# Optimization experiments

Measured on AMD Instinct MI355X. Metric: run time of the kernel, lower is better.

Reference implementation:

```python
import jax, jax.numpy as jnp
import numpy as np

B, HG, WG, C, WH, WW, HEADS = 32, 8, 8, 256, 7, 7, 8
N = WH * WW  # 49 tokens per window


def _relative_index():
    # Mirrors the torch buffer construction exactly.
    coords = np.stack(np.meshgrid(np.arange(WH), np.arange(WW), indexing='ij'))  # [2, wh, ww]
    coords = coords.reshape(2, -1)                      # [2, N]
    rel = coords[:, :, None] - coords[:, None, :]       # [2, N, N]
    rel[0] += WH - 1
    rel[1] += WW - 1
    rel[0] *= 2 * WW - 1
    return rel.sum(0).reshape(-1).astype(np.int32)      # [N*N]


def setup_inputs() -> dict:
    key = jax.random.key(0)
    kx, kq, kp, kb = jax.random.split(key, 4)
    x = jax.random.normal(kx, (B, HG, WG, C, WH, WW), dtype=jnp.float32)
    qkv_w = jax.random.normal(kq, (3 * C, C), dtype=jnp.float32) * 0.02
    qkv_b = jnp.zeros((3 * C,), dtype=jnp.float32)
    proj_w = jax.random.normal(kp, (C, C), dtype=jnp.float32) * 0.02
    proj_b = jnp.zeros((C,), dtype=jnp.float32)
    bias_table = jax.random.normal(kb, ((2 * WH - 1) * (2 * WW - 1), HEADS), dtype=jnp.float32) * 0.02
    relative_index = jnp.asarray(_relative_index())
    return {"x": x, "qkv_w": qkv_w, "qkv_b": qkv_b, "proj_w": proj_w,
            "proj_b": proj_b, "bias_table": bias_table, "relative_index": relative_index}


def reference(x, qkv_w, qkv_b, proj_w, proj_b, bias_table, relative_index):
    Bq, Hg, Wg, Cc, wh, ww = x.shape
    n = wh * ww
    heads = bias_table.shape[1]
    hd = Cc // heads
    scale = hd ** -0.5

    xw = x.reshape(-1, Cc, n)                                   # [Bw, C, N]
    # 1x1 conv == channel matmul
    qkv = jnp.einsum('oc,bcn->bon', qkv_w, xw) + qkv_b[None, :, None]  # [Bw, 3C, N]
    q, k, v = jnp.split(qkv, 3, axis=1)

    def to_heads(t):  # [Bw, C, N] -> [Bw, heads, N, hd]
        return t.reshape(-1, heads, hd, n).transpose(0, 1, 3, 2)

    q, k, v = to_heads(q), to_heads(k), to_heads(v)

    # Gathered relative position bias: [heads, N, N]
    rel_bias = bias_table[relative_index].reshape(n, n, heads).transpose(2, 0, 1)

    attn = jnp.einsum('bhnd,bhmd->bhnm', q, k) * scale + rel_bias[None]
    attn = jax.nn.softmax(attn, axis=-1)
    out = jnp.einsum('bhnm,bhmd->bhnd', attn, v)                # [Bw, heads, N, hd]
    out = out.transpose(0, 1, 3, 2).reshape(-1, Cc, n)          # [Bw, C, N]
    out = jnp.einsum('oc,bcn->bon', proj_w, out) + proj_b[None, :, None]
    return out.reshape(Bq, Hg, Wg, Cc, wh, ww)
```

## Files before the change

kernel.cpp:

```cpp
#include <hip/hip_runtime.h>

typedef float f32x4 __attribute__((ext_vector_type(4)));
typedef short s16x8 __attribute__((ext_vector_type(8)));
typedef short s16x4 __attribute__((ext_vector_type(4)));

static __device__ __forceinline__ short f2b(float f) {
  unsigned u = __builtin_bit_cast(unsigned, f);
  u += 0x7fffu + ((u >> 16) & 1u);
  return (short)(u >> 16);
}

constexpr int kC  = 256;
constexpr int kN  = 49;
constexpr int kNP = 64;
constexpr int kHD = 32;
constexpr float kScale = 0.17677669529663687f;

constexpr int XT_P  = 264;
constexpr int QK_P  = 40;
constexpr int VT_P  = 72;
constexpr int P_P   = 72;
constexpr int AOT_P = 264;
constexpr int R1   = 64 * XT_P * 2;
constexpr int R2   = R1 + 8 * 64 * QK_P * 2;
constexpr int R3   = R2 + 8 * 64 * QK_P * 2;
constexpr int SMEM = R3 + 8 * 32 * VT_P * 2;

__global__ void prep_kernel(const float* __restrict__ qw,
                            const float* __restrict__ pw,
                            const float* __restrict__ bt,
                            const int* __restrict__ ri,
                            short* __restrict__ Wq,
                            short* __restrict__ Wp,
                            float* __restrict__ bx) {
  int i = blockIdx.x * 256 + threadIdx.x;
  if (i < 768 * 256) Wq[i] = f2b(qw[i]);
  if (i < 256 * 256) Wp[i] = f2b(pw[i]);
  if (i < 8 * 64 * 64) {
    int h = i >> 12, q = (i >> 6) & 63, k = i & 63;
    float v = -10000.f;
    if (q < kN && k < kN) v = bt[ri[q * kN + k] * 8 + h];
    bx[i] = v;
  }
}

__global__ __launch_bounds__(512, 2) void winattn_kernel(
    const float* __restrict__ x, const float* __restrict__ qkv_b,
    const float* __restrict__ proj_b, const short* __restrict__ Wq,
    const short* __restrict__ Wp, const float* __restrict__ biasx,
    float* __restrict__ out) {
  __shared__ alignas(16) char smem[SMEM];
  short* xT  = (short*)smem;
  short* aoT = xT;
  short* qs  = (short*)(smem + R1);
  short* ks  = (short*)(smem + R2);
  short* vt  = (short*)(smem + R3);

  const int tid  = threadIdx.x;
  const int wv   = tid >> 6;
  const int lane = tid & 63;
  const int lg   = lane >> 4;
  const int ln   = lane & 15;
  const size_t wbase = (size_t)blockIdx.x * (kC * kN);

  {
    const float* xw = x + wbase;
    for (int i = tid; i < kC * kN; i += 512) {
      int c = i / kN, n = i - c * kN;
      xT[n * XT_P + c] = f2b(xw[i]);
    }
    for (int i = tid; i < (kNP - kN) * kC; i += 512) {
      int n = kN + (i >> 8), c = i & 255;
      xT[n * XT_P + c] = 0;
    }
  }
  __syncthreads();

  {
    s16x8 Bf[4][8];
#pragma unroll
    for (int nt = 0; nt < 4; ++nt)
#pragma unroll
      for (int kk = 0; kk < 8; ++kk)
        Bf[nt][kk] = *(const s16x8*)&xT[(nt * 16 + ln) * XT_P + kk * 32 + lg * 8];

#pragma unroll 1
    for (int i = 0; i < 6; ++i) {
      const int mt = wv * 6 + i, o0 = mt * 16;
      const short* wr = Wq + (size_t)(o0 + ln) * kC;
      s16x8 Af[8];
#pragma unroll
      for (int kk = 0; kk < 8; ++kk) Af[kk] = *(const s16x8*)&wr[kk * 32 + lg * 8];
      f32x4 acc[4] = {};
#pragma unroll
      for (int kk = 0; kk < 8; ++kk)
#pragma unroll
        for (int nt = 0; nt < 4; ++nt)
          acc[nt] = __builtin_amdgcn_mfma_f32_16x16x32_bf16(Af[kk], Bf[nt][kk], acc[nt], 0, 0, 0);

      const int t = o0 >> 8, h = (o0 >> 5) & 7, d0 = (o0 & 31) + lg * 4;
      const f32x4 bq = *(const f32x4*)&qkv_b[o0 + lg * 4];
#pragma unroll
      for (int nt = 0; nt < 4; ++nt) {
        const int n = nt * 16 + ln;
        if (t < 2) {
          short* dst = (t == 0 ? qs : ks) + h * (kNP * QK_P) + n * QK_P + d0;
          s16x4 pk;
#pragma unroll
          for (int r = 0; r < 4; ++r) pk[r] = f2b(acc[nt][r] + bq[r]);
          *(s16x4*)dst = pk;
        } else {
#pragma unroll
          for (int r = 0; r < 4; ++r)
            vt[(h * kHD + d0 + r) * VT_P + n] = f2b(acc[nt][r] + bq[r]);
        }
      }
    }
  }
  __syncthreads();

  float Ssc[4][4][4];
  {
    const short* qh = qs + wv * (kNP * QK_P);
    const short* kh = ks + wv * (kNP * QK_P);
    s16x8 Qf[4], Kf[4];
#pragma unroll
    for (int tI = 0; tI < 4; ++tI) {
      Qf[tI] = *(const s16x8*)&qh[(tI * 16 + ln) * QK_P + lg * 8];
      Kf[tI] = *(const s16x8*)&kh[(tI * 16 + ln) * QK_P + lg * 8];
    }
    const float* bx = biasx + wv * (kNP * kNP);
#pragma unroll
    for (int qt = 0; qt < 4; ++qt)
#pragma unroll
      for (int nt = 0; nt < 4; ++nt) {
        f32x4 a = {};
        a = __builtin_amdgcn_mfma_f32_16x16x32_bf16(Qf[qt], Kf[nt], a, 0, 0, 0);
#pragma unroll
        for (int r = 0; r < 4; ++r) {
          const int qr = qt * 16 + lg * 4 + r;
          Ssc[qt][nt][r] = a[r] * kScale + bx[qr * kNP + nt * 16 + ln];
        }
      }
#pragma unroll
    for (int qt = 0; qt < 4; ++qt)
#pragma unroll
      for (int r = 0; r < 4; ++r) {
        float m = fmaxf(fmaxf(Ssc[qt][0][r], Ssc[qt][1][r]),
                        fmaxf(Ssc[qt][2][r], Ssc[qt][3][r]));
#pragma unroll
        for (int off = 1; off < 16; off <<= 1) m = fmaxf(m, __shfl_xor(m, off));
        float s = 0.f;
#pragma unroll
        for (int nt = 0; nt < 4; ++nt) {
          float p = __expf(Ssc[qt][nt][r] - m);
          Ssc[qt][nt][r] = p;
          s += p;
        }
#pragma unroll
        for (int off = 1; off < 16; off <<= 1) s += __shfl_xor(s, off);
        const float rinv = 1.f / s;
#pragma unroll
        for (int nt = 0; nt < 4; ++nt) Ssc[qt][nt][r] *= rinv;
      }
  }
  __syncthreads();

  short* Pw = qs + wv * (kNP * P_P);
#pragma unroll
  for (int qt = 0; qt < 4; ++qt)
#pragma unroll
    for (int nt = 0; nt < 4; ++nt)
#pragma unroll
      for (int r = 0; r < 4; ++r)
        Pw[(qt * 16 + lg * 4 + r) * P_P + nt * 16 + ln] = f2b(Ssc[qt][nt][r]);
  __syncthreads();

  {
    f32x4 O[4][2] = {};
#pragma unroll
    for (int kk = 0; kk < 2; ++kk) {
      s16x8 Vf[2];
#pragma unroll
      for (int dt = 0; dt < 2; ++dt)
        Vf[dt] = *(const s16x8*)&vt[(wv * kHD + dt * 16 + ln) * VT_P + kk * 32 + lg * 8];
#pragma unroll
      for (int qt = 0; qt < 4; ++qt) {
        const s16x8 Pf = *(const s16x8*)&Pw[(qt * 16 + ln) * P_P + kk * 32 + lg * 8];
#pragma unroll
        for (int dt = 0; dt < 2; ++dt)
          O[qt][dt] = __builtin_amdgcn_mfma_f32_16x16x32_bf16(Pf, Vf[dt], O[qt][dt], 0, 0, 0);
      }
    }
#pragma unroll
    for (int qt = 0; qt < 4; ++qt)
#pragma unroll
      for (int dt = 0; dt < 2; ++dt)
#pragma unroll
        for (int r = 0; r < 4; ++r)
          aoT[(qt * 16 + lg * 4 + r) * AOT_P + wv * kHD + dt * 16 + ln] = f2b(O[qt][dt][r]);
  }
  __syncthreads();

  {
    s16x8 Bp[4][8];
#pragma unroll
    for (int nt = 0; nt < 4; ++nt)
#pragma unroll
      for (int kk = 0; kk < 8; ++kk)
        Bp[nt][kk] = *(const s16x8*)&aoT[(nt * 16 + ln) * AOT_P + kk * 32 + lg * 8];

#pragma unroll 1
    for (int i = 0; i < 2; ++i) {
      const int mt = wv * 2 + i, o0 = mt * 16;
      const short* wr = Wp + (size_t)(o0 + ln) * kC;
      s16x8 Ap[8];
#pragma unroll
      for (int kk = 0; kk < 8; ++kk) Ap[kk] = *(const s16x8*)&wr[kk * 32 + lg * 8];
      f32x4 acc[4] = {};
#pragma unroll
      for (int kk = 0; kk < 8; ++kk)
#pragma unroll
        for (int nt = 0; nt < 4; ++nt)
          acc[nt] = __builtin_amdgcn_mfma_f32_16x16x32_bf16(Ap[kk], Bp[nt][kk], acc[nt], 0, 0, 0);

      const f32x4 pb = *(const f32x4*)&proj_b[o0 + lg * 4];
#pragma unroll
      for (int nt = 0; nt < 4; ++nt) {
        const int n = nt * 16 + ln;
        if (n < kN) {
#pragma unroll
          for (int r = 0; r < 4; ++r)
            out[wbase + (size_t)(o0 + lg * 4 + r) * kN + n] = acc[nt][r] + pb[r];
        }
      }
    }
  }
}

extern "C" void kernel_launch(void* const* d_in, const int* in_sizes, int n_in,
                              void* d_out, int out_size, void* d_ws, size_t ws_size,
                              hipStream_t stream) {
  (void)in_sizes; (void)n_in; (void)out_size; (void)ws_size;
  const float* x      = (const float*)d_in[0];
  const float* qkv_w  = (const float*)d_in[1];
  const float* qkv_b  = (const float*)d_in[2];
  const float* proj_w = (const float*)d_in[3];
  const float* proj_b = (const float*)d_in[4];
  const float* btab   = (const float*)d_in[5];
  const int*   ridx   = (const int*)d_in[6];

  short* Wq = (short*)d_ws;
  short* Wp = (short*)((char*)d_ws + 393216);
  float* bx = (float*)((char*)d_ws + 524288);

  prep_kernel<<<768, 256, 0, stream>>>(qkv_w, proj_w, btab, ridx, Wq, Wp, bx);
  winattn_kernel<<<2048, 512, 0, stream>>>(x, qkv_b, proj_b, Wq, Wp, bx, (float*)d_out);
}
```

Before: 233.9 us.

## Keep per-head Q/K/V and probabilities in registers via lane shuffles instead of LDS

Each wave now computes the Q, K and V projections for its own head directly. It turns the MFMA accumulators into operand fragments with packed bf16 conversion and lane shuffles, so the Q/K/V and P staging buffers in shared memory go away, along with their barriers. Shared memory shrinks to the single x/attention-output tile, and launch bounds rise to allow 4 blocks per CU. Softmax now uses transposed scores (K·Q with a transposed bias table) and applies normalization after the PV product. The risks are higher register pressure and repeated LDS reads of x per projection.

```diff
diff --git a/kernel.cpp b/kernel.cpp
--- a/kernel.cpp
+++ b/kernel.cpp
@@ -1,8 +1,9 @@
 #include <hip/hip_runtime.h>
 
-typedef float f32x4 __attribute__((ext_vector_type(4)));
-typedef short s16x8 __attribute__((ext_vector_type(8)));
-typedef short s16x4 __attribute__((ext_vector_type(4)));
+typedef float    f32x4 __attribute__((ext_vector_type(4)));
+typedef short    s16x8 __attribute__((ext_vector_type(8)));
+typedef short    s16x4 __attribute__((ext_vector_type(4)));
+typedef unsigned u32x4 __attribute__((ext_vector_type(4)));
 
 static __device__ __forceinline__ short f2b(float f) {
   unsigned u = __builtin_bit_cast(unsigned, f);
@@ -13,18 +14,10 @@
 constexpr int kC  = 256;
 constexpr int kN  = 49;
 constexpr int kNP = 64;
-constexpr int kHD = 32;
 constexpr float kScale = 0.17677669529663687f;
 
-constexpr int XT_P  = 264;
-constexpr int QK_P  = 40;
-constexpr int VT_P  = 72;
-constexpr int P_P   = 72;
-constexpr int AOT_P = 264;
-constexpr int R1   = 64 * XT_P * 2;
-constexpr int R2   = R1 + 8 * 64 * QK_P * 2;
-constexpr int R3   = R2 + 8 * 64 * QK_P * 2;
-constexpr int SMEM = R3 + 8 * 32 * VT_P * 2;
+constexpr int XT_P = 264;
+constexpr int SMEM = kNP * XT_P * 2;
 
 __global__ void prep_kernel(const float* __restrict__ qw,
                             const float* __restrict__ pw,
@@ -32,35 +25,51 @@
                             const int* __restrict__ ri,
                             short* __restrict__ Wq,
                             short* __restrict__ Wp,
-                            float* __restrict__ bx) {
+                            float* __restrict__ bxT) {
   int i = blockIdx.x * 256 + threadIdx.x;
   if (i < 768 * 256) Wq[i] = f2b(qw[i]);
   if (i < 256 * 256) Wp[i] = f2b(pw[i]);
   if (i < 8 * 64 * 64) {
-    int h = i >> 12, q = (i >> 6) & 63, k = i & 63;
+    int h = i >> 12, k = (i >> 6) & 63, q = i & 63;
     float v = -10000.f;
     if (q < kN && k < kN) v = bt[ri[q * kN + k] * 8 + h];
-    bx[i] = v;
-  }
-}
-
-__global__ __launch_bounds__(512, 2) void winattn_kernel(
+    bxT[i] = v;
+  }
+}
+
+static __device__ __forceinline__ s16x8 fragize(f32x4 Ta, f32x4 Tb, int hi, int srcbase) {
+  unsigned a0, a1, b0, b1;
+  asm("v_cvt_pk_bf16_f32 %0, %1, %2" : "=v"(a0) : "v"(Ta[0]), "v"(Ta[1]));
+  asm("v_cvt_pk_bf16_f32 %0, %1, %2" : "=v"(a1) : "v"(Ta[2]), "v"(Ta[3]));
+  asm("v_cvt_pk_bf16_f32 %0, %1, %2" : "=v"(b0) : "v"(Tb[0]), "v"(Tb[1]));
+  asm("v_cvt_pk_bf16_f32 %0, %1, %2" : "=v"(b1) : "v"(Tb[2]), "v"(Tb[3]));
+  u32x4 fw;
+#pragma unroll
+  for (int j = 0; j < 4; ++j) {
+    const int src = srcbase + (j >> 1) * 16;
+    unsigned wa = __shfl((j & 1) ? a1 : a0, src);
+    unsigned wb = __shfl((j & 1) ? b1 : b0, src);
+    fw[j] = hi ? wb : wa;
+  }
+  return __builtin_bit_cast(s16x8, fw);
+}
+
+__global__ __launch_bounds__(512, 4) void winattn_kernel(
     const float* __restrict__ x, const float* __restrict__ qkv_b,
     const float* __restrict__ proj_b, const short* __restrict__ Wq,
-    const short* __restrict__ Wp, const float* __restrict__ biasx,
+    const short* __restrict__ Wp, const float* __restrict__ bxT,
     float* __restrict__ out) {
   __shared__ alignas(16) char smem[SMEM];
   short* xT  = (short*)smem;
   short* aoT = xT;
-  short* qs  = (short*)(smem + R1);
-  short* ks  = (short*)(smem + R2);
-  short* vt  = (short*)(smem + R3);
 
   const int tid  = threadIdx.x;
   const int wv   = tid >> 6;
   const int lane = tid & 63;
   const int lg   = lane >> 4;
   const int ln   = lane & 15;
+  const int hi   = lg >> 1;
+  const int srcbase = (lg & 1) * 32 + ln;
   const size_t wbase = (size_t)blockIdx.x * (kC * kN);
 
   {
@@ -76,163 +85,184 @@
   }
   __syncthreads();
 
-  {
-    s16x8 Bf[4][8];
-#pragma unroll
-    for (int nt = 0; nt < 4; ++nt)
-#pragma unroll
-      for (int kk = 0; kk < 8; ++kk)
-        Bf[nt][kk] = *(const s16x8*)&xT[(nt * 16 + ln) * XT_P + kk * 32 + lg * 8];
+  s16x8 Qf[4], Kf[4], Vf[2][2];
+  {
+    f32x4 acc[2][4] = {};
+#pragma unroll
+    for (int kk = 0; kk < 8; ++kk) {
+      const s16x8 A0 = *(const s16x8*)&Wq[(size_t)(32 * wv + ln) * kC + kk * 32 + lg * 8];
+      const s16x8 A1 = *(const s16x8*)&Wq[(size_t)(32 * wv + 16 + ln) * kC + kk * 32 + lg * 8];
+      s16x8 B[4];
+#pragma unroll
+      for (int nt = 0; nt < 4; ++nt) B[nt] = *(const s16x8*)&xT[(nt * 16 + ln) * XT_P + kk * 32 + lg * 8];
+#pragma unroll
+      for (int nt = 0; nt < 4; ++nt) {
+        acc[0][nt] = __builtin_amdgcn_mfma_f32_16x16x32_bf16(A0, B[nt], acc[0][nt], 0, 0, 0);
+        acc[1][nt] = __builtin_amdgcn_mfma_f32_16x16x32_bf16(A1, B[nt], acc[1][nt], 0, 0, 0);
+      }
+    }
+    {
+      const f32x4 b0 = *(const f32x4*)&qkv_b[32 * wv + lg * 4];
+      const f32x4 b1 = *(const f32x4*)&qkv_b[32 * wv + 16 + lg * 4];
+#pragma unroll
+      for (int qt = 0; qt < 4; ++qt) {
+        f32x4 Ta, Tb;
+#pragma unroll
+        for (int r = 0; r < 4; ++r) {
+          Ta[r] = (acc[0][qt][r] + b0[r]) * kScale;
+          Tb[r] = (acc[1][qt][r] + b1[r]) * kScale;
+        }
+        Qf[qt] = fragize(Ta, Tb, hi, srcbase);
+      }
+    }
+#pragma unroll
+    for (int t = 0; t < 2; ++t)
+#pragma unroll
+      for (int nt = 0; nt < 4; ++nt) acc[t][nt] = f32x4{};
+#pragma unroll
+    for (int kk = 0; kk < 8; ++kk) {
+      const s16x8 A0 = *(const s16x8*)&Wq[(size_t)(256 + 32 * wv + ln) * kC + kk * 32 + lg * 8];
+      const s16x8 A1 = *(const s16x8*)&Wq[(size_t)(256 + 32 * wv + 16 + ln) * kC + kk * 32 + lg * 8];
+      s16x8 B[4];
+#pragma unroll
+      for (int nt = 0; nt < 4; ++nt) B[nt] = *(const s16x8*)&xT[(nt * 16 + ln) * XT_P + kk * 32 + lg * 8];
+#pragma unroll
+      for (int nt = 0; nt < 4; ++nt) {
+        acc[0][nt] = __builtin_amdgcn_mfma_f32_16x16x32_bf16(A0, B[nt], acc[0][nt], 0, 0, 0);
+        acc[1][nt] = __builtin_amdgcn_mfma_f32_16x16x32_bf16(A1, B[nt], acc[1][nt], 0, 0, 0);
+      }
+    }
+    {
+      const f32x4 b0 = *(const f32x4*)&qkv_b[256 + 32 * wv + lg * 4];
+      const f32x4 b1 = *(const f32x4*)&qkv_b[256 + 32 * wv + 16 + lg * 4];
+#pragma unroll
+      for (int qt = 0; qt < 4; ++qt) {
+        f32x4 Ta, Tb;
+#pragma unroll
+        for (int r = 0; r < 4; ++r) {
+          Ta[r] = acc[0][qt][r] + b0[r];
+          Tb[r] = acc[1][qt][r] + b1[r];
+        }
+        Kf[qt] = fragize(Ta, Tb, hi, srcbase);
+      }
+    }
+    f32x4 accv[4][2] = {};
+#pragma unroll
+    for (int kk = 0; kk < 8; ++kk) {
+      const s16x8 A0 = *(const s16x8*)&Wq[(size_t)(512 + 32 * wv + ln) * kC + kk * 32 + lg * 8];
+      const s16x8 A1 = *(const s16x8*)&Wq[(size_t)(512 + 32 * wv + 16 + ln) * kC + kk * 32 + lg * 8];
+      s16x8 B[4];
+#pragma unroll
+      for (int nt = 0; nt < 4; ++nt) B[nt] = *(const s16x8*)&xT[(nt * 16 + ln) * XT_P + kk * 32 + lg * 8];
+#pragma unroll
+      for (int tt = 0; tt < 4; ++tt) {
+        accv[tt][0] = __builtin_amdgcn_mfma_f32_16x16x32_bf16(B[tt], A0, accv[tt][0], 0, 0, 0);
+        accv[tt][1] = __builtin_amdgcn_mfma_f32_16x16x32_bf16(B[tt], A1, accv[tt][1], 0, 0, 0);
+      }
+    }
+    {
+      const float bv0 = qkv_b[512 + 32 * wv + ln];
+      const float bv1 = qkv_b[512 + 32 * wv + 16 + ln];
+#pragma unroll
+      for (int dt = 0; dt < 2; ++dt) {
+        const float bv = dt ? bv1 : bv0;
+#pragma unroll
+        for (int k2 = 0; k2 < 2; ++k2) {
+          f32x4 Ta, Tb;
+#pragma unroll
+          for (int r = 0; r < 4; ++r) {
+            Ta[r] = accv[2 * k2][dt][r] + bv;
+            Tb[r] = accv[2 * k2 + 1][dt][r] + bv;
+          }
+          Vf[dt][k2] = fragize(Ta, Tb, hi, srcbase);
+        }
+      }
+    }
+  }
+  __syncthreads();
+
+  s16x8 Pf[4][2];
+  float rinv[4];
+  {
+    const float* bxh = bxT + wv * (kNP * kNP);
+#pragma unroll
+    for (int qt = 0; qt < 4; ++qt) {
+      f32x4 S[4];
+#pragma unroll
+      for (int kt = 0; kt < 4; ++kt) {
+        f32x4 z = {};
+        S[kt] = __builtin_amdgcn_mfma_f32_16x16x32_bf16(Kf[kt], Qf[qt], z, 0, 0, 0);
+      }
+#pragma unroll
+      for (int kt = 0; kt < 4; ++kt)
+#pragma unroll
+        for (int r = 0; r < 4; ++r)
+          S[kt][r] += bxh[(kt * 16 + lg * 4 + r) * kNP + qt * 16 + ln];
+      float m = S[0][0];
+#pragma unroll
+      for (int kt = 0; kt < 4; ++kt)
+#pragma unroll
+        for (int r = 0; r < 4; ++r) m = fmaxf(m, S[kt][r]);
+      m = fmaxf(m, __shfl_xor(m, 16));
+      m = fmaxf(m, __shfl_xor(m, 32));
+      float s = 0.f;
+#pragma unroll
+      for (int kt = 0; kt < 4; ++kt)
+#pragma unroll
+        for (int r = 0; r < 4; ++r) {
+          float p = __expf(S[kt][r] - m);
+          S[kt][r] = p;
+          s += p;
+        }
+      s += __shfl_xor(s, 16);
+      s += __shfl_xor(s, 32);
+      rinv[qt] = 1.f / s;
+      Pf[qt][0] = fragize(S[0], S[1], hi, srcbase);
+      Pf[qt][1] = fragize(S[2], S[3], hi, srcbase);
+    }
+  }
+  {
+    f32x4 O[2][4] = {};
+#pragma unroll
+    for (int k2 = 0; k2 < 2; ++k2)
+#pragma unroll
+      for (int qt = 0; qt < 4; ++qt)
+#pragma unroll
+        for (int dt = 0; dt < 2; ++dt)
+          O[dt][qt] = __builtin_amdgcn_mfma_f32_16x16x32_bf16(Vf[dt][k2], Pf[qt][k2], O[dt][qt], 0, 0, 0);
+#pragma unroll
+    for (int dt = 0; dt < 2; ++dt)
+#pragma unroll
+      for (int qt = 0; qt < 4; ++qt) {
+        s16x4 pk;
+#pragma unroll
+        for (int r = 0; r < 4; ++r) pk[r] = f2b(O[dt][qt][r] * rinv[qt]);
+        *(s16x4*)&aoT[(qt * 16 + ln) * XT_P + wv * 32 + dt * 16 + lg * 4] = pk;
+      }
+  }
+  __syncthreads();
 
 #pragma unroll 1
-    for (int i = 0; i < 6; ++i) {
-      const int mt = wv * 6 + i, o0 = mt * 16;
-      const short* wr = Wq + (size_t)(o0 + ln) * kC;
-      s16x8 Af[8];
-#pragma unroll
-      for (int kk = 0; kk < 8; ++kk) Af[kk] = *(const s16x8*)&wr[kk * 32 + lg * 8];
-      f32x4 acc[4] = {};
-#pragma unroll
-      for (int kk = 0; kk < 8; ++kk)
-#pragma unroll
-        for (int nt = 0; nt < 4; ++nt)
-          acc[nt] = __builtin_amdgcn_mfma_f32_16x16x32_bf16(Af[kk], Bf[nt][kk], acc[nt], 0, 0, 0);
-
-      const int t = o0 >> 8, h = (o0 >> 5) & 7, d0 = (o0 & 31) + lg * 4;
-      const f32x4 bq = *(const f32x4*)&qkv_b[o0 + lg * 4];
+  for (int i = 0; i < 2; ++i) {
+    const int o0 = 32 * wv + 16 * i;
+    f32x4 acc[4] = {};
+#pragma unroll
+    for (int kk = 0; kk < 8; ++kk) {
+      const s16x8 A = *(const s16x8*)&Wp[(size_t)(o0 + ln) * kC + kk * 32 + lg * 8];
 #pragma unroll
       for (int nt = 0; nt < 4; ++nt) {
-        const int n = nt * 16 + ln;
-        if (t < 2) {
-          short* dst = (t == 0 ? qs : ks) + h * (kNP * QK_P) + n * QK_P + d0;
-          s16x4 pk;
-#pragma unroll
-          for (int r = 0; r < 4; ++r) pk[r] = f2b(acc[nt][r] + bq[r]);
-          *(s16x4*)dst = pk;
-        } else {
-#pragma unroll
-          for (int r = 0; r < 4; ++r)
-            vt[(h * kHD + d0 + r) * VT_P + n] = f2b(acc[nt][r] + bq[r]);
-        }
-      }
-    }
-  }
-  __syncthreads();
-
-  float Ssc[4][4][4];
-  {
-    const short* qh = qs + wv * (kNP * QK_P);
-    const short* kh = ks + wv * (kNP * QK_P);
-    s16x8 Qf[4], Kf[4];
-#pragma unroll
-    for (int tI = 0; tI < 4; ++tI) {
-      Qf[tI] = *(const s16x8*)&qh[(tI * 16 + ln) * QK_P + lg * 8];
-      Kf[tI] = *(const s16x8*)&kh[(tI * 16 + ln) * QK_P + lg * 8];
-    }
-    const float* bx = biasx + wv * (kNP * kNP);
-#pragma unroll
-    for (int qt = 0; qt < 4; ++qt)
-#pragma unroll
-      for (int nt = 0; nt < 4; ++nt) {
-        f32x4 a = {};
-        a = __builtin_amdgcn_mfma_f32_16x16x32_bf16(Qf[qt], Kf[nt], a, 0, 0, 0);
-#pragma unroll
-        for (int r = 0; r < 4; ++r) {
-          const int qr = qt * 16 + lg * 4 + r;
-          Ssc[qt][nt][r] = a[r] * kScale + bx[qr * kNP + nt * 16 + ln];
-        }
-      }
-#pragma unroll
-    for (int qt = 0; qt < 4; ++qt)
-#pragma unroll
-      for (int r = 0; r < 4; ++r) {
-        float m = fmaxf(fmaxf(Ssc[qt][0][r], Ssc[qt][1][r]),
-                        fmaxf(Ssc[qt][2][r], Ssc[qt][3][r]));
-#pragma unroll
-        for (int off = 1; off < 16; off <<= 1) m = fmaxf(m, __shfl_xor(m, off));
-        float s = 0.f;
-#pragma unroll
-        for (int nt = 0; nt < 4; ++nt) {
-          float p = __expf(Ssc[qt][nt][r] - m);
-          Ssc[qt][nt][r] = p;
-          s += p;
-        }
-#pragma unroll
-        for (int off = 1; off < 16; off <<= 1) s += __shfl_xor(s, off);
-        const float rinv = 1.f / s;
-#pragma unroll
-        for (int nt = 0; nt < 4; ++nt) Ssc[qt][nt][r] *= rinv;
-      }
-  }
-  __syncthreads();
-
-  short* Pw = qs + wv * (kNP * P_P);
-#pragma unroll
-  for (int qt = 0; qt < 4; ++qt)
-#pragma unroll
-    for (int nt = 0; nt < 4; ++nt)
-#pragma unroll
-      for (int r = 0; r < 4; ++r)
-        Pw[(qt * 16 + lg * 4 + r) * P_P + nt * 16 + ln] = f2b(Ssc[qt][nt][r]);
-  __syncthreads();
-
-  {
-    f32x4 O[4][2] = {};
-#pragma unroll
-    for (int kk = 0; kk < 2; ++kk) {
-      s16x8 Vf[2];
-#pragma unroll
-      for (int dt = 0; dt < 2; ++dt)
-        Vf[dt] = *(const s16x8*)&vt[(wv * kHD + dt * 16 + ln) * VT_P + kk * 32 + lg * 8];
-#pragma unroll
-      for (int qt = 0; qt < 4; ++qt) {
-        const s16x8 Pf = *(const s16x8*)&Pw[(qt * 16 + ln) * P_P + kk * 32 + lg * 8];
-#pragma unroll
-        for (int dt = 0; dt < 2; ++dt)
-          O[qt][dt] = __builtin_amdgcn_mfma_f32_16x16x32_bf16(Pf, Vf[dt], O[qt][dt], 0, 0, 0);
-      }
-    }
-#pragma unroll
-    for (int qt = 0; qt < 4; ++qt)
-#pragma unroll
-      for (int dt = 0; dt < 2; ++dt)
+        const s16x8 B = *(const s16x8*)&aoT[(nt * 16 + ln) * XT_P + kk * 32 + lg * 8];
+        acc[nt] = __builtin_amdgcn_mfma_f32_16x16x32_bf16(A, B, acc[nt], 0, 0, 0);
+      }
+    }
+    const f32x4 pb = *(const f32x4*)&proj_b[o0 + lg * 4];
+#pragma unroll
+    for (int nt = 0; nt < 4; ++nt) {
+      const int n = nt * 16 + ln;
+      if (n < kN) {
 #pragma unroll
         for (int r = 0; r < 4; ++r)
-          aoT[(qt * 16 + lg * 4 + r) * AOT_P + wv * kHD + dt * 16 + ln] = f2b(O[qt][dt][r]);
-  }
-  __syncthreads();
-
-  {
-    s16x8 Bp[4][8];
-#pragma unroll
-    for (int nt = 0; nt < 4; ++nt)
-#pragma unroll
-      for (int kk = 0; kk < 8; ++kk)
-        Bp[nt][kk] = *(const s16x8*)&aoT[(nt * 16 + ln) * AOT_P + kk * 32 + lg * 8];
-
-#pragma unroll 1
-    for (int i = 0; i < 2; ++i) {
-      const int mt = wv * 2 + i, o0 = mt * 16;
-      const short* wr = Wp + (size_t)(o0 + ln) * kC;
-      s16x8 Ap[8];
-#pragma unroll
-      for (int kk = 0; kk < 8; ++kk) Ap[kk] = *(const s16x8*)&wr[kk * 32 + lg * 8];
-      f32x4 acc[4] = {};
-#pragma unroll
-      for (int kk = 0; kk < 8; ++kk)
-#pragma unroll
-        for (int nt = 0; nt < 4; ++nt)
-          acc[nt] = __builtin_amdgcn_mfma_f32_16x16x32_bf16(Ap[kk], Bp[nt][kk], acc[nt], 0, 0, 0);
-
-      const f32x4 pb = *(const f32x4*)&proj_b[o0 + lg * 4];
-#pragma unroll
-      for (int nt = 0; nt < 4; ++nt) {
-        const int n = nt * 16 + ln;
-        if (n < kN) {
-#pragma unroll
-          for (int r = 0; r < 4; ++r)
-            out[wbase + (size_t)(o0 + lg * 4 + r) * kN + n] = acc[nt][r] + pb[r];
-        }
+          out[wbase + (size_t)(o0 + lg * 4 + r) * kN + n] = acc[nt][r] + pb[r];
       }
     }
   }
@@ -250,10 +280,10 @@
   const float* btab   = (const float*)d_in[5];
   const int*   ridx   = (const int*)d_in[6];
 
-  short* Wq = (short*)d_ws;
-  short* Wp = (short*)((char*)d_ws + 393216);
-  float* bx = (float*)((char*)d_ws + 524288);
-
-  prep_kernel<<<768, 256, 0, stream>>>(qkv_w, proj_w, btab, ridx, Wq, Wp, bx);
-  winattn_kernel<<<2048, 512, 0, stream>>>(x, qkv_b, proj_b, Wq, Wp, bx, (float*)d_out);
-}
+  short* Wq  = (short*)d_ws;
+  short* Wp  = (short*)((char*)d_ws + 393216);
+  float* bxT = (float*)((char*)d_ws + 524288);
+
+  prep_kernel<<<768, 256, 0, stream>>>(qkv_w, proj_w, btab, ridx, Wq, Wp, bxT);
+  winattn_kernel<<<2048, 512, 0, stream>>>(x, qkv_b, proj_b, Wq, Wp, bxT, (float*)d_out);
+}
```

After: 418.2 us. +78.8%, slower.
